# Kernel tuning notes

Measured on AMD Instinct MI355X. Metric: run time of the kernel, lower is better.

The kernel has to match this reference:

```python
import jax, jax.numpy as jnp
import numpy as np

N, E, H, ED, NF, NG = 75000, 150000, 44, 10, 15000, 1500


def _seg_mean(v, idx, n):
    s = jax.ops.segment_sum(v, idx, num_segments=n)
    c = jax.ops.segment_sum(jnp.ones((v.shape[0], 1), v.dtype), idx, num_segments=n)
    return s / jnp.maximum(c, 1.0)


def setup_inputs() -> dict:
    key = jax.random.key(0)
    ks = jax.random.split(key, 26)
    p = lambda k, shape: (jax.random.normal(k, shape, dtype=jnp.float32) * 0.1)
    x = jax.random.normal(ks[0], (N, H), dtype=jnp.float32)
    edge_index = jax.random.randint(ks[1], (2, E), 0, N)
    edge_attr = jax.random.normal(ks[2], (E, ED), dtype=jnp.float32)
    node2frag = (jnp.arange(N) * NF) // N          # sorted, covers all fragments
    frag2graph = (jnp.arange(NF) * NG) // NF       # sorted, covers all graphs
    noise = jax.random.normal(ks[3], (NF, H), dtype=jnp.float32)
    return {
        "x": x, "edge_attr": edge_attr, "noise": noise,
        "W0": p(ks[4], (H, H)), "b0": jnp.zeros((H,)),
        "We1": p(ks[5], (ED, ED)), "be1": jnp.zeros((ED,)),
        "We2": p(ks[6], (ED, H * H)), "be2": jnp.zeros((H * H,)),
        "root": p(ks[7], (H, H)), "conv_b": jnp.zeros((H,)),
        "Wm": p(ks[8], (2 * H, H)), "bm": jnp.zeros((H,)),
        "Wc1": p(ks[9], (H, H)), "bc1": jnp.zeros((H,)),
        "bn_g": jnp.ones((H,)), "bn_b": jnp.zeros((H,)),
        "Wc2": p(ks[10], (H, 1)), "bc2": jnp.zeros((1,)),
        "Wp1": p(ks[11], (H, 256)), "bp1": jnp.zeros((256,)),
        "Wp2": p(ks[12], (256, 128)), "bp2": jnp.zeros((128,)),
        "Wp3": p(ks[13], (128, 1)), "bp3": jnp.zeros((1,)),
        "edge_index": edge_index, "node2frag": node2frag, "frag2graph": frag2graph,
        "n_frags": NF, "n_graphs": NG,
    }


def reference(x, edge_attr, noise, W0, b0, We1, be1, We2, be2, root, conv_b, Wm, bm,
              Wc1, bc1, bn_g, bn_b, Wc2, bc2, Wp1, bp1, Wp2, bp2, Wp3, bp3,
              edge_index, node2frag, frag2graph, n_frags, n_graphs):
    n, h = x.shape
    init = x
    out = jax.nn.relu(x @ W0 + b0)
    # edge-conditioned weight matrices (computed once; edge_attr is fixed)
    ew = (jax.nn.relu(edge_attr @ We1 + be1) @ We2 + be2).reshape(-1, h, h)  # [E,h,h]
    src, dst = edge_index[0], edge_index[1]
    for _ in range(3):  # num_step_message_passing
        msg = jnp.einsum('eh,eho->eo', out[src], ew)               # per-edge matvec
        agg = jax.ops.segment_sum(msg, dst, num_segments=n)        # aggr='add'
        m = jax.nn.relu(agg + out @ root + conv_b)                 # NNConv + relu
        out = jnp.concatenate([m, out], axis=1) @ Wm + bm          # message_layer
    nodef = out + init
    # F.normalize(dim=1)
    nodef = nodef / jnp.maximum(jnp.linalg.norm(nodef, axis=1, keepdims=True), 1e-12)
    frag = _seg_mean(nodef, node2frag, n_frags)                    # global_mean_pool
    # compressor: Linear -> BatchNorm(train stats) -> ReLU -> Linear -> Sigmoid
    z = frag @ Wc1 + bc1
    z = (z - z.mean(0)) / jnp.sqrt(z.var(0) + 1e-5) * bn_g + bn_b
    w = jax.nn.sigmoid(jax.nn.relu(z) @ Wc2 + bc2).squeeze(-1)     # [NF]
    lp = w[:, None]
    ln = 1.0 - lp
    preserve_rate = (w > 0.5).astype(jnp.float32).mean()
    static = jax.lax.stop_gradient(frag)
    cnt = jax.ops.segment_sum(jnp.ones((n_frags,), jnp.float32), frag2graph, num_segments=n_graphs)[:, None]
    gsum = jax.ops.segment_sum(static, frag2graph, num_segments=n_graphs)
    gmean = gsum / jnp.maximum(cnt, 1.0)
    gsq = jax.ops.segment_sum(static * static, frag2graph, num_segments=n_graphs)
    gvar = (gsq - cnt * gmean * gmean) / jnp.maximum(cnt - 1.0, 1.0)  # unbiased (scatter_std)
    gstd = jnp.sqrt(jnp.maximum(gvar, 0.0))
    mean_f = gmean[frag2graph]
    std_f = gstd[frag2graph]
    nmean = lp * frag + ln * mean_f
    nstd = ln * std_f
    noisy = nmean + noise * nstd
    sub = _seg_mean(noisy, frag2graph, n_graphs)
    pred = jax.nn.sigmoid(jax.nn.relu(jax.nn.relu(sub @ Wp1 + bp1) @ Wp2 + bp2) @ Wp3 + bp3)
    eps = 1e-7
    kl = 0.5 * jax.ops.segment_sum((nstd ** 2 / (std_f + eps) ** 2).mean(axis=1), frag2graph, num_segments=n_graphs)[:, None] \
         + jax.ops.segment_sum(((nmean - mean_f) / (std_f + eps)) ** 2, frag2graph, num_segments=n_graphs)
    return pred, kl.mean(), preserve_rate
```

## Files before the change

kernel.cpp:

```cpp
#include <hip/hip_runtime.h>
#include <math.h>

#define NN 75000
#define NE 150000
#define H 44
#define HH 1936
#define EDIM 10
#define NFRAG 15000
#define NGRAPH 1500

typedef const float* __restrict__ cfp;
typedef float* __restrict__ fpt;
typedef const int* __restrict__ cip;
typedef int* __restrict__ ipt;

__device__ __forceinline__ float relu_(float v){ return v > 0.f ? v : 0.f; }
__device__ __forceinline__ float sigmoid_(float v){ return 1.f/(1.f + expf(-v)); }

__global__ __launch_bounds__(256) void k_hist(cip ei, ipt cnt){
    int e = blockIdx.x*256 + threadIdx.x;
    if(e>=NE) return;
    atomicAdd(&cnt[ei[NE+e]], 1);
}

__global__ __launch_bounds__(1024) void k_scan1(cip cnt, ipt incl, ipt bsum){
    __shared__ int sd[1024];
    int i = blockIdx.x*1024 + threadIdx.x;
    int v = (i<NN)? cnt[i] : 0;
    sd[threadIdx.x]=v;
    __syncthreads();
    for(int off=1; off<1024; off<<=1){
        int t = (threadIdx.x>=off)? sd[threadIdx.x-off] : 0;
        __syncthreads();
        sd[threadIdx.x]+=t;
        __syncthreads();
    }
    if(i<NN) incl[i]=sd[threadIdx.x];
    if(threadIdx.x==1023) bsum[blockIdx.x]=sd[1023];
}

__global__ void k_scan2(ipt bsum, int nblk){
    if(threadIdx.x==0 && blockIdx.x==0){
        int run=0;
        for(int b=0;b<nblk;b++){ int t=bsum[b]; bsum[b]=run; run+=t; }
    }
}

__global__ __launch_bounds__(1024) void k_scan3(cip incl, cip bsum, ipt rowptr){
    int i = blockIdx.x*1024 + threadIdx.x;
    if(i==0) rowptr[0]=0;
    if(i<NN) rowptr[i+1] = incl[i] + bsum[i>>10];
}

__global__ __launch_bounds__(256) void k_scatter(cip ei, cip rowptr, ipt cur, ipt eidx){
    int e = blockIdx.x*256 + threadIdx.x;
    if(e>=NE) return;
    int d = ei[NE+e];
    int pos = rowptr[d] + atomicAdd(&cur[d],1);
    eidx[pos]=e;
}

__global__ __launch_bounds__(256) void k_in(cfp x, cfp W0, cfp b0, fpt out){
    __shared__ float sW[HH];
    __shared__ float sb[H];
    for(int i=threadIdx.x;i<HH;i+=256) sW[i]=W0[i];
    if(threadIdx.x<H) sb[threadIdx.x]=b0[threadIdx.x];
    __syncthreads();
    int n = blockIdx.x*256 + threadIdx.x;
    if(n>=NN) return;
    float xv[H];
    const float4* xp = (const float4*)(x + (size_t)n*H);
    #pragma unroll
    for(int i=0;i<11;i++){ float4 v=xp[i]; xv[4*i]=v.x; xv[4*i+1]=v.y; xv[4*i+2]=v.z; xv[4*i+3]=v.w; }
    float acc[H];
    #pragma unroll
    for(int o=0;o<H;o++) acc[o]=sb[o];
    #pragma unroll
    for(int h=0;h<H;h++){
        float xh = xv[h];
        const float4* wr = (const float4*)(sW + h*H);
        #pragma unroll
        for(int o=0;o<11;o++){
            float4 w = wr[o];
            acc[4*o]+=xh*w.x; acc[4*o+1]+=xh*w.y; acc[4*o+2]+=xh*w.z; acc[4*o+3]+=xh*w.w;
        }
    }
    float4* op = (float4*)(out + (size_t)n*H);
    #pragma unroll
    for(int i=0;i<11;i++) op[i] = make_float4(relu_(acc[4*i]),relu_(acc[4*i+1]),relu_(acc[4*i+2]),relu_(acc[4*i+3]));
}

__global__ __launch_bounds__(256) void k_b2(cfp out, cfp be2, fpt b2){
    __shared__ float sB[HH];
    for(int i=threadIdx.x;i<HH;i+=256) sB[i]=be2[i];
    __syncthreads();
    int n = blockIdx.x*256 + threadIdx.x;
    if(n>=NN) return;
    float ov[H];
    const float4* op = (const float4*)(out + (size_t)n*H);
    #pragma unroll
    for(int i=0;i<11;i++){ float4 v=op[i]; ov[4*i]=v.x; ov[4*i+1]=v.y; ov[4*i+2]=v.z; ov[4*i+3]=v.w; }
    float acc[H];
    #pragma unroll
    for(int o=0;o<H;o++) acc[o]=0.f;
    #pragma unroll
    for(int h=0;h<H;h++){
        float oh = ov[h];
        const float4* wr = (const float4*)(sB + h*H);
        #pragma unroll
        for(int o=0;o<11;o++){
            float4 w = wr[o];
            acc[4*o]+=oh*w.x; acc[4*o+1]+=oh*w.y; acc[4*o+2]+=oh*w.z; acc[4*o+3]+=oh*w.w;
        }
    }
    float4* bp = (float4*)(b2 + (size_t)n*H);
    #pragma unroll
    for(int i=0;i<11;i++) bp[i] = make_float4(acc[4*i],acc[4*i+1],acc[4*i+2],acc[4*i+3]);
}

__global__ __launch_bounds__(256) void k_edge(cfp ea, cfp We1, cfp be1, fpt t){
    __shared__ float sW[EDIM*EDIM];
    __shared__ float sb[EDIM];
    if(threadIdx.x<EDIM*EDIM) sW[threadIdx.x]=We1[threadIdx.x];
    if(threadIdx.x<EDIM) sb[threadIdx.x]=be1[threadIdx.x];
    __syncthreads();
    int e = blockIdx.x*256 + threadIdx.x;
    if(e>=NE) return;
    float acc[EDIM];
    #pragma unroll
    for(int j=0;j<EDIM;j++) acc[j]=sb[j];
    #pragma unroll
    for(int k=0;k<EDIM;k++){
        float a = ea[(size_t)e*EDIM + k];
        #pragma unroll
        for(int j=0;j<EDIM;j++) acc[j]+=a*sW[k*EDIM+j];
    }
    #pragma unroll
    for(int j=0;j<EDIM;j++) t[(size_t)e*EDIM+j]=relu_(acc[j]);
}

__global__ __launch_bounds__(256,2) void k_msg2(cfp out, cfp b2, cfp t, cfp We2, cip ei, fpt msgbuf){
    __shared__ float4 sW[EDIM*HH/4];
    const float4* wg = (const float4*)We2;
    for(int i=threadIdx.x;i<EDIM*HH/4;i+=256) sW[i]=wg[i];
    __syncthreads();
    int e0 = blockIdx.x*256 + threadIdx.x;
    if(e0 >= NE/2) return;
    int e1 = e0 + NE/2;
    int s0 = ei[e0], s1 = ei[e1];
    float ov0[H], ov1[H];
    const float4* p0 = (const float4*)(out + (size_t)s0*H);
    const float4* p1 = (const float4*)(out + (size_t)s1*H);
    #pragma unroll
    for(int i=0;i<11;i++){
        float4 a=p0[i]; ov0[4*i]=a.x; ov0[4*i+1]=a.y; ov0[4*i+2]=a.z; ov0[4*i+3]=a.w;
        float4 b=p1[i]; ov1[4*i]=b.x; ov1[4*i+1]=b.y; ov1[4*i+2]=b.z; ov1[4*i+3]=b.w;
    }
    float4 m0[11], m1[11];
    const float4* q0 = (const float4*)(b2 + (size_t)s0*H);
    const float4* q1 = (const float4*)(b2 + (size_t)s1*H);
    #pragma unroll
    for(int i=0;i<11;i++){ m0[i]=q0[i]; m1[i]=q1[i]; }
    for(int k=0;k<EDIM;k++){
        float t0 = t[(size_t)e0*EDIM + k];
        float t1 = t[(size_t)e1*EDIM + k];
        const float4* wrow = &sW[k*(HH/4)];
        #pragma unroll
        for(int h=0;h<H;h++){
            float z0 = t0*ov0[h];
            float z1 = t1*ov1[h];
            #pragma unroll
            for(int o=0;o<11;o++){
                float4 w = wrow[h*11+o];
                m0[o].x+=z0*w.x; m0[o].y+=z0*w.y; m0[o].z+=z0*w.z; m0[o].w+=z0*w.w;
                m1[o].x+=z1*w.x; m1[o].y+=z1*w.y; m1[o].z+=z1*w.z; m1[o].w+=z1*w.w;
            }
        }
    }
    float4* w0 = (float4*)(msgbuf + (size_t)e0*H);
    float4* w1 = (float4*)(msgbuf + (size_t)e1*H);
    #pragma unroll
    for(int o=0;o<11;o++){ w0[o]=m0[o]; w1[o]=m1[o]; }
}

__global__ __launch_bounds__(256,2) void k_comb(cfp out, cfp msgbuf, cip rowptr, cip eidx,
                                                cfp root, cfp conv_b, cfp Wm, cfp bm, fpt out_nxt){
    __shared__ float sR[HH];
    __shared__ float sM[2*HH];
    __shared__ float scb[H];
    __shared__ float sbm[H];
    for(int i=threadIdx.x;i<HH;i+=256) sR[i]=root[i];
    for(int i=threadIdx.x;i<2*HH;i+=256) sM[i]=Wm[i];
    if(threadIdx.x<H){ scb[threadIdx.x]=conv_b[threadIdx.x]; sbm[threadIdx.x]=bm[threadIdx.x]; }
    __syncthreads();
    int n = blockIdx.x*256 + threadIdx.x;
    if(n>=NN) return;
    float m[H];
    #pragma unroll
    for(int o=0;o<H;o++) m[o]=scb[o];
    int st = rowptr[n], en = rowptr[n+1];
    for(int j=st;j<en;j++){
        int e = eidx[j];
        const float4* mp = (const float4*)(msgbuf + (size_t)e*H);
        #pragma unroll
        for(int i=0;i<11;i++){
            float4 v=mp[i];
            m[4*i]+=v.x; m[4*i+1]+=v.y; m[4*i+2]+=v.z; m[4*i+3]+=v.w;
        }
    }
    float ov[H];
    const float4* op = (const float4*)(out + (size_t)n*H);
    #pragma unroll
    for(int i=0;i<11;i++){ float4 v=op[i]; ov[4*i]=v.x; ov[4*i+1]=v.y; ov[4*i+2]=v.z; ov[4*i+3]=v.w; }
    #pragma unroll
    for(int h=0;h<H;h++){
        float oh = ov[h];
        const float4* wr = (const float4*)(sR + h*H);
        #pragma unroll
        for(int o=0;o<11;o++){
            float4 w=wr[o];
            m[4*o]+=oh*w.x; m[4*o+1]+=oh*w.y; m[4*o+2]+=oh*w.z; m[4*o+3]+=oh*w.w;
        }
    }
    #pragma unroll
    for(int o=0;o<H;o++) m[o]=relu_(m[o]);
    float no[H];
    #pragma unroll
    for(int o=0;o<H;o++) no[o]=sbm[o];
    #pragma unroll
    for(int h=0;h<H;h++){
        float mh = m[h];
        float oh = ov[h];
        const float4* w1 = (const float4*)(sM + h*H);
        const float4* w2 = (const float4*)(sM + (H+h)*H);
        #pragma unroll
        for(int o=0;o<11;o++){
            float4 a=w1[o], b=w2[o];
            no[4*o]+=mh*a.x+oh*b.x; no[4*o+1]+=mh*a.y+oh*b.y; no[4*o+2]+=mh*a.z+oh*b.z; no[4*o+3]+=mh*a.w+oh*b.w;
        }
    }
    float4* np_ = (float4*)(out_nxt + (size_t)n*H);
    #pragma unroll
    for(int i=0;i<11;i++) np_[i]=make_float4(no[4*i],no[4*i+1],no[4*i+2],no[4*i+3]);
}

__global__ __launch_bounds__(256) void k_frag(cfp out, cfp x, cfp Wc1, cfp bc1,
                                              fpt frag, fpt z, fpt colstat){
    __shared__ float sW[HH];
    __shared__ float sb[H];
    for(int i=threadIdx.x;i<HH;i+=256) sW[i]=Wc1[i];
    if(threadIdx.x<H) sb[threadIdx.x]=bc1[threadIdx.x];
    __syncthreads();
    int f = blockIdx.x*256 + threadIdx.x;
    bool valid = f < NFRAG;
    int fc = valid ? f : NFRAG-1;
    float fr[H];
    #pragma unroll
    for(int o=0;o<H;o++) fr[o]=0.f;
    for(int j=0;j<5;j++){
        int n = 5*fc + j;
        float v[H]; float ss=0.f;
        const float4* op=(const float4*)(out + (size_t)n*H);
        const float4* xp=(const float4*)(x + (size_t)n*H);
        #pragma unroll
        for(int i=0;i<11;i++){
            float4 a=op[i], b=xp[i];
            v[4*i]=a.x+b.x; v[4*i+1]=a.y+b.y; v[4*i+2]=a.z+b.z; v[4*i+3]=a.w+b.w;
        }
        #pragma unroll
        for(int o=0;o<H;o++) ss+=v[o]*v[o];
        float inv = 1.f/fmaxf(sqrtf(ss),1e-12f);
        #pragma unroll
        for(int o=0;o<H;o++) fr[o]+=v[o]*inv;
    }
    #pragma unroll
    for(int o=0;o<H;o++) fr[o]*=0.2f;
    float zr[H];
    #pragma unroll
    for(int o=0;o<H;o++) zr[o]=sb[o];
    #pragma unroll
    for(int h=0;h<H;h++){
        float fh = fr[h];
        const float4* wr=(const float4*)(sW + h*H);
        #pragma unroll
        for(int o=0;o<11;o++){
            float4 w=wr[o];
            zr[4*o]+=fh*w.x; zr[4*o+1]+=fh*w.y; zr[4*o+2]+=fh*w.z; zr[4*o+3]+=fh*w.w;
        }
    }
    if(valid){
        float4* fw=(float4*)(frag+(size_t)f*H);
        float4* zw=(float4*)(z+(size_t)f*H);
        #pragma unroll
        for(int i=0;i<11;i++){
            fw[i]=make_float4(fr[4*i],fr[4*i+1],fr[4*i+2],fr[4*i+3]);
            zw[i]=make_float4(zr[4*i],zr[4*i+1],zr[4*i+2],zr[4*i+3]);
        }
    }
    #pragma unroll
    for(int o=0;o<H;o++){
        float s = valid ? zr[o] : 0.f;
        float q = s*s;
        #pragma unroll
        for(int dlt=32;dlt>0;dlt>>=1){ s+=__shfl_xor(s,dlt); q+=__shfl_xor(q,dlt); }
        if((threadIdx.x&63)==0){ atomicAdd(colstat+o,s); atomicAdd(colstat+H+o,q); }
    }
}

__global__ __launch_bounds__(256) void k_bnw(cfp z, cfp colstat, cfp bng, cfp bnb, cfp Wc2, cfp bc2, fpt w, fpt pres){
    int f = blockIdx.x*256 + threadIdx.x;
    bool valid = f < NFRAG;
    int fc = valid ? f : NFRAG-1;
    float s = 0.f;
    #pragma unroll
    for(int o=0;o<H;o++){
        float mean = colstat[o]*(1.f/NFRAG);
        float var  = colstat[H+o]*(1.f/NFRAG) - mean*mean;
        float zb = (z[(size_t)fc*H+o]-mean)*rsqrtf(var+1e-5f)*bng[o]+bnb[o];
        s += relu_(zb)*Wc2[o];
    }
    float wv = sigmoid_(s + bc2[0]);
    if(valid) w[f]=wv;
    unsigned long long msk = __ballot(valid && (wv > 0.5f));
    if((threadIdx.x&63)==0) atomicAdd(pres,(float)__popcll(msk));
}

__global__ __launch_bounds__(64) void k_graph(cfp frag, cfp w, cfp noise, fpt sub, fpt klg){
    int g = blockIdx.x;
    int o = threadIdx.x;
    bool act = o < H;
    int oc = act ? o : 0;
    float frv[10];
    #pragma unroll
    for(int j=0;j<10;j++) frv[j] = act ? frag[(size_t)(10*g+j)*H + oc] : 0.f;
    float gs=0.f, gq=0.f;
    #pragma unroll
    for(int j=0;j<10;j++){ gs+=frv[j]; gq+=frv[j]*frv[j]; }
    float gmean = gs*0.1f;
    float gvar  = (gq - 10.f*gmean*gmean)*(1.f/9.f);
    float gstd  = sqrtf(fmaxf(gvar,0.f));
    float se    = gstd + 1e-7f;
    float c     = act ? (gstd/se)*(gstd/se) : 0.f;
    float C = c;
    #pragma unroll
    for(int dlt=32;dlt>0;dlt>>=1) C+=__shfl_xor(C,dlt);
    float subacc=0.f, B=0.f, Sln=0.f;
    #pragma unroll
    for(int j=0;j<10;j++){
        float lp = w[10*g+j];
        float ln = 1.f-lp;
        Sln += ln*ln;
        float nm = lp*frv[j] + ln*gmean;
        float ns = ln*gstd;
        float ny = nm + (act ? noise[(size_t)(10*g+j)*H + oc] : 0.f)*ns;
        subacc += ny;
        float dd = (nm-gmean)/se;
        B += dd*dd;
    }
    if(act) sub[(size_t)g*H+o] = subacc*0.1f;
    float Bv = act ? B : 0.f;
    #pragma unroll
    for(int dlt=32;dlt>0;dlt>>=1) Bv+=__shfl_xor(Bv,dlt);
    if(o==0) klg[g] = 0.5f*C*Sln + Bv;
}

__global__ __launch_bounds__(256) void k_pred(cfp sub, cfp Wp1, cfp bp1, cfp Wp2, cfp bp2,
                                              cfp Wp3, cfp bp3, fpt outp){
    __shared__ float ssub[H];
    __shared__ float sh1[256];
    __shared__ float sh2[128];
    int g = blockIdx.x; int tid = threadIdx.x;
    if(tid<H) ssub[tid] = sub[(size_t)g*H+tid];
    __syncthreads();
    float a = bp1[tid];
    for(int o=0;o<H;o++) a += ssub[o]*Wp1[(size_t)o*256+tid];
    sh1[tid]=relu_(a);
    __syncthreads();
    if(tid<128){
        float b = bp2[tid];
        for(int i=0;i<256;i++) b += sh1[i]*Wp2[(size_t)i*128+tid];
        sh2[tid]=relu_(b);
    }
    __syncthreads();
    if(tid<64){
        float s = sh2[tid]*Wp3[tid] + sh2[tid+64]*Wp3[tid+64];
        #pragma unroll
        for(int dlt=32;dlt>0;dlt>>=1) s+=__shfl_xor(s,dlt);
        if(tid==0) outp[g]=sigmoid_(s+bp3[0]);
    }
}

__global__ void k_final(cfp klg, cfp pres, fpt outp){
    float s = 0.f;
    for(int i=threadIdx.x;i<NGRAPH;i+=256) s+=klg[i];
    __shared__ float red[4];
    #pragma unroll
    for(int dlt=32;dlt>0;dlt>>=1) s+=__shfl_xor(s,dlt);
    int wid = threadIdx.x>>6;
    if((threadIdx.x&63)==0) red[wid]=s;
    __syncthreads();
    if(threadIdx.x==0){
        float tot = red[0]+red[1]+red[2]+red[3];
        outp[NGRAPH]   = tot/(float)(NGRAPH*H);
        outp[NGRAPH+1] = pres[0]/(float)NFRAG;
    }
}

extern "C" void kernel_launch(void* const* d_in, const int* in_sizes, int n_in,
                              void* d_out, int out_size, void* d_ws, size_t ws_size,
                              hipStream_t stream) {
    (void)in_sizes; (void)n_in; (void)out_size; (void)ws_size;
    const float* x        =(const float*)d_in[0];
    const float* edge_attr=(const float*)d_in[1];
    const float* noise    =(const float*)d_in[2];
    const float* W0       =(const float*)d_in[3];
    const float* b0       =(const float*)d_in[4];
    const float* We1      =(const float*)d_in[5];
    const float* be1      =(const float*)d_in[6];
    const float* We2      =(const float*)d_in[7];
    const float* be2      =(const float*)d_in[8];
    const float* root     =(const float*)d_in[9];
    const float* conv_b   =(const float*)d_in[10];
    const float* Wm       =(const float*)d_in[11];
    const float* bm       =(const float*)d_in[12];
    const float* Wc1      =(const float*)d_in[13];
    const float* bc1      =(const float*)d_in[14];
    const float* bng      =(const float*)d_in[15];
    const float* bnb      =(const float*)d_in[16];
    const float* Wc2      =(const float*)d_in[17];
    const float* bc2      =(const float*)d_in[18];
    const float* Wp1      =(const float*)d_in[19];
    const float* bp1      =(const float*)d_in[20];
    const float* Wp2      =(const float*)d_in[21];
    const float* bp2      =(const float*)d_in[22];
    const float* Wp3      =(const float*)d_in[23];
    const float* bp3      =(const float*)d_in[24];
    const int*   ei       =(const int*)d_in[25];

    float* ws = (float*)d_ws;
    const size_t NH = (size_t)NN*H;
    float* out_a  = ws;
    float* out_b  = out_a + NH;
    float* b2_a   = out_b + NH;
    float* b2_b   = b2_a + NH;
    float* tbuf   = b2_b + NH;
    float* msgbuf = tbuf + (size_t)NE*EDIM;
    float* frag   = msgbuf + (size_t)NE*H;
    float* zbuf   = frag + (size_t)NFRAG*H;
    float* wv     = zbuf + (size_t)NFRAG*H;
    float* sub    = wv + NFRAG;
    float* klg    = sub + (size_t)NGRAPH*H;
    int*   rowptr = (int*)(klg + NGRAPH);
    int*   eidx   = rowptr + (NN+1);
    int*   bsum   = eidx + NE;
    int*   incl   = bsum + 128;
    int*   cnt    = incl + NN;
    int*   cur    = cnt + NN;
    float* colstat= (float*)(cur + NN);
    float* pres   = colstat + 2*H;

    hipMemsetAsync(cnt, 0, (size_t)(2*NN + 2*H + 8)*sizeof(float), stream);

    const int nb_n = (NN + 255)/256;
    const int nb_e = (NE + 255)/256;
    const int nb_h = (NE/2 + 255)/256;
    const int nb_f = (NFRAG + 255)/256;
    const int nblk = (NN + 1023)/1024;

    k_hist   <<<nb_e,256,0,stream>>>(ei, cnt);
    k_scan1  <<<nblk,1024,0,stream>>>(cnt, incl, bsum);
    k_scan2  <<<1,64,0,stream>>>(bsum, nblk);
    k_scan3  <<<nblk,1024,0,stream>>>(incl, bsum, rowptr);
    k_scatter<<<nb_e,256,0,stream>>>(ei, rowptr, cur, eidx);

    k_in  <<<nb_n,256,0,stream>>>(x, W0, b0, out_a);
    k_b2  <<<nb_n,256,0,stream>>>(out_a, be2, b2_a);
    k_edge<<<nb_e,256,0,stream>>>(edge_attr, We1, be1, tbuf);

    float* cur_o = out_a; float* cur_b = b2_a;
    float* nxt_o = out_b; float* nxt_b = b2_b;
    for(int it=0; it<3; ++it){
        k_msg2<<<nb_h,256,0,stream>>>(cur_o, cur_b, tbuf, We2, ei, msgbuf);
        k_comb<<<nb_n,256,0,stream>>>(cur_o, msgbuf, rowptr, eidx, root, conv_b, Wm, bm, nxt_o);
        if(it<2) k_b2<<<nb_n,256,0,stream>>>(nxt_o, be2, nxt_b);
        float* tp;
        tp=cur_o; cur_o=nxt_o; nxt_o=tp;
        tp=cur_b; cur_b=nxt_b; nxt_b=tp;
    }

    k_frag <<<nb_f,256,0,stream>>>(cur_o, x, Wc1, bc1, frag, zbuf, colstat);
    k_bnw  <<<nb_f,256,0,stream>>>(zbuf, colstat, bng, bnb, Wc2, bc2, wv, pres);
    k_graph<<<NGRAPH,64,0,stream>>>(frag, wv, noise, sub, klg);
    k_pred <<<NGRAPH,256,0,stream>>>(sub, Wp1, bp1, Wp2, bp2, Wp3, bp3, (float*)d_out);
    k_final<<<1,256,0,stream>>>(klg, pres, (float*)d_out);
}
```

Before: 1.410 ms.

## Restructure node/edge matmuls with padded rows, LDS-transposed tiles, and output-group split

Node feature rows are padded to 48 floats, in four 11-wide groups of 12, and the per-thread 44x44 dense loops in k_b2, k_msg and k_comb become block-cooperative kernels. Each block stages its tile transposed in LDS. Each wavefront computes one 11-output group for four (or two) rows, reading weights from global/scalar memory instead of per-thread register rows. The aim is lower register pressure and better reuse of the weight stream. k_frag is also split so that normalization, fragment pooling and the Wc1 matmul are done cooperatively in LDS, with 4 threads per fragment. The cost is extra LDS traffic, more synchronisation and padded memory footprint.

```diff
diff --git a/kernel.cpp b/kernel.cpp
--- a/kernel.cpp
+++ b/kernel.cpp
@@ -4,7 +4,7 @@
 #define NN 75000
 #define NE 150000
 #define H 44
-#define HH 1936
+#define HS 48
 #define EDIM 10
 #define NFRAG 15000
 #define NGRAPH 1500
@@ -14,8 +14,8 @@
 typedef const int* __restrict__ cip;
 typedef int* __restrict__ ipt;
 
-__device__ __forceinline__ float relu_(float v){ return v > 0.f ? v : 0.f; }
-__device__ __forceinline__ float sigmoid_(float v){ return 1.f/(1.f + expf(-v)); }
+__device__ __forceinline__ float relu_(float v){ return v>0.f?v:0.f; }
+__device__ __forceinline__ float sigmoid_(float v){ return 1.f/(1.f+expf(-v)); }
 
 __global__ __launch_bounds__(256) void k_hist(cip ei, ipt cnt){
     int e = blockIdx.x*256 + threadIdx.x;
@@ -61,9 +61,9 @@
 }
 
 __global__ __launch_bounds__(256) void k_in(cfp x, cfp W0, cfp b0, fpt out){
-    __shared__ float sW[HH];
+    __shared__ float sW[H*H];
     __shared__ float sb[H];
-    for(int i=threadIdx.x;i<HH;i+=256) sW[i]=W0[i];
+    for(int i=threadIdx.x;i<H*H;i+=256) sW[i]=W0[i];
     if(threadIdx.x<H) sb[threadIdx.x]=b0[threadIdx.x];
     __syncthreads();
     int n = blockIdx.x*256 + threadIdx.x;
@@ -85,37 +85,60 @@
             acc[4*o]+=xh*w.x; acc[4*o+1]+=xh*w.y; acc[4*o+2]+=xh*w.z; acc[4*o+3]+=xh*w.w;
         }
     }
-    float4* op = (float4*)(out + (size_t)n*H);
-    #pragma unroll
-    for(int i=0;i<11;i++) op[i] = make_float4(relu_(acc[4*i]),relu_(acc[4*i+1]),relu_(acc[4*i+2]),relu_(acc[4*i+3]));
-}
-
-__global__ __launch_bounds__(256) void k_b2(cfp out, cfp be2, fpt b2){
-    __shared__ float sB[HH];
-    for(int i=threadIdx.x;i<HH;i+=256) sB[i]=be2[i];
-    __syncthreads();
-    int n = blockIdx.x*256 + threadIdx.x;
-    if(n>=NN) return;
-    float ov[H];
-    const float4* op = (const float4*)(out + (size_t)n*H);
-    #pragma unroll
-    for(int i=0;i<11;i++){ float4 v=op[i]; ov[4*i]=v.x; ov[4*i+1]=v.y; ov[4*i+2]=v.z; ov[4*i+3]=v.w; }
-    float acc[H];
-    #pragma unroll
-    for(int o=0;o<H;o++) acc[o]=0.f;
+    #pragma unroll
+    for(int o=0;o<H;o++) acc[o]=relu_(acc[o]);
+    float* row = out + (size_t)n*HS;
+    #pragma unroll
+    for(int s=0;s<4;s++){
+        float4* p=(float4*)(row + s*12);
+        p[0]=make_float4(acc[11*s+0],acc[11*s+1],acc[11*s+2],acc[11*s+3]);
+        p[1]=make_float4(acc[11*s+4],acc[11*s+5],acc[11*s+6],acc[11*s+7]);
+        p[2]=make_float4(acc[11*s+8],acc[11*s+9],acc[11*s+10],0.f);
+    }
+}
+
+#define NB2 256
+__global__ __launch_bounds__(256,3) void k_b2(cfp out, cfp be2, fpt b2){
+    __shared__ float ovT[HS*NB2];
+    int tid=threadIdx.x, lane=tid&63;
+    int og = __builtin_amdgcn_readfirstlane(tid>>6);
+    size_t base=(size_t)blockIdx.x*NB2;
+    { size_t n=base+tid; size_t nc = n<NN? n : NN-1;
+      const float4* orow=(const float4*)(out + nc*HS);
+      #pragma unroll
+      for(int i=0;i<12;i++){ float4 v=orow[i];
+        ovT[(4*i+0)*NB2+tid]=v.x; ovT[(4*i+1)*NB2+tid]=v.y;
+        ovT[(4*i+2)*NB2+tid]=v.z; ovT[(4*i+3)*NB2+tid]=v.w; }
+    }
+    __syncthreads();
+    float m[4][11];
+    #pragma unroll
+    for(int j=0;j<4;j++)
+        #pragma unroll
+        for(int o=0;o<11;o++) m[j][o]=0.f;
+    const float* wog = be2 + og*11;
     #pragma unroll
     for(int h=0;h<H;h++){
-        float oh = ov[h];
-        const float4* wr = (const float4*)(sB + h*H);
+        int hl = h + h/11;
+        const float4* ovp=(const float4*)(ovT + hl*NB2 + lane*4);
+        float4 ov=ovp[0];
         #pragma unroll
         for(int o=0;o<11;o++){
-            float4 w = wr[o];
-            acc[4*o]+=oh*w.x; acc[4*o+1]+=oh*w.y; acc[4*o+2]+=oh*w.z; acc[4*o+3]+=oh*w.w;
-        }
-    }
-    float4* bp = (float4*)(b2 + (size_t)n*H);
-    #pragma unroll
-    for(int i=0;i<11;i++) bp[i] = make_float4(acc[4*i],acc[4*i+1],acc[4*i+2],acc[4*i+3]);
+            float w = wog[h*H+o];
+            m[0][o]+=ov.x*w; m[1][o]+=ov.y*w; m[2][o]+=ov.z*w; m[3][o]+=ov.w*w;
+        }
+    }
+    size_t n0 = base + (size_t)lane*4;
+    #pragma unroll
+    for(int j=0;j<4;j++){
+        size_t n=n0+j;
+        if(n<NN){
+            float4* p=(float4*)(b2 + n*HS + og*12);
+            p[0]=make_float4(m[j][0],m[j][1],m[j][2],m[j][3]);
+            p[1]=make_float4(m[j][4],m[j][5],m[j][6],m[j][7]);
+            p[2]=make_float4(m[j][8],m[j][9],m[j][10],0.f);
+        }
+    }
 }
 
 __global__ __launch_bounds__(256) void k_edge(cfp ea, cfp We1, cfp be1, fpt t){
@@ -139,171 +162,230 @@
     for(int j=0;j<EDIM;j++) t[(size_t)e*EDIM+j]=relu_(acc[j]);
 }
 
-__global__ __launch_bounds__(256,2) void k_msg2(cfp out, cfp b2, cfp t, cfp We2, cip ei, fpt msgbuf){
-    __shared__ float4 sW[EDIM*HH/4];
-    const float4* wg = (const float4*)We2;
-    for(int i=threadIdx.x;i<EDIM*HH/4;i+=256) sW[i]=wg[i];
-    __syncthreads();
-    int e0 = blockIdx.x*256 + threadIdx.x;
-    if(e0 >= NE/2) return;
-    int e1 = e0 + NE/2;
-    int s0 = ei[e0], s1 = ei[e1];
-    float ov0[H], ov1[H];
-    const float4* p0 = (const float4*)(out + (size_t)s0*H);
-    const float4* p1 = (const float4*)(out + (size_t)s1*H);
-    #pragma unroll
-    for(int i=0;i<11;i++){
-        float4 a=p0[i]; ov0[4*i]=a.x; ov0[4*i+1]=a.y; ov0[4*i+2]=a.z; ov0[4*i+3]=a.w;
-        float4 b=p1[i]; ov1[4*i]=b.x; ov1[4*i+1]=b.y; ov1[4*i+2]=b.z; ov1[4*i+3]=b.w;
-    }
-    float4 m0[11], m1[11];
-    const float4* q0 = (const float4*)(b2 + (size_t)s0*H);
-    const float4* q1 = (const float4*)(b2 + (size_t)s1*H);
-    #pragma unroll
-    for(int i=0;i<11;i++){ m0[i]=q0[i]; m1[i]=q1[i]; }
+#define EBM 256
+__global__ __launch_bounds__(256,2) void k_msg(cfp out, cfp b2, cfp t, cfp We2, cip ei, fpt msg){
+    __shared__ float ovT[HS*EBM];
+    __shared__ float tT[EDIM*EBM];
+    int tid=threadIdx.x, lane=tid&63;
+    int og = __builtin_amdgcn_readfirstlane(tid>>6);
+    size_t base=(size_t)blockIdx.x*EBM;
+    { size_t e=base+tid; size_t ec = e<NE? e : NE-1;
+      int s = ei[ec];
+      const float4* orow=(const float4*)(out + (size_t)s*HS);
+      #pragma unroll
+      for(int i=0;i<12;i++){ float4 v=orow[i];
+        ovT[(4*i+0)*EBM+tid]=v.x; ovT[(4*i+1)*EBM+tid]=v.y;
+        ovT[(4*i+2)*EBM+tid]=v.z; ovT[(4*i+3)*EBM+tid]=v.w; }
+      const float2* trow=(const float2*)(t + ec*EDIM);
+      #pragma unroll
+      for(int i=0;i<5;i++){ float2 v=trow[i]; tT[(2*i+0)*EBM+tid]=v.x; tT[(2*i+1)*EBM+tid]=v.y; }
+    }
+    __syncthreads();
+    size_t e0 = base + (size_t)lane*4;
+    int srcj[4];
+    #pragma unroll
+    for(int j=0;j<4;j++){ size_t e=e0+j; srcj[j]=ei[e<NE? e : NE-1]; }
+    float m[4][11];
+    #pragma unroll
+    for(int j=0;j<4;j++){
+        const float4* br=(const float4*)(b2 + (size_t)srcj[j]*HS + og*12);
+        float4 A=br[0],B=br[1],C=br[2];
+        m[j][0]=A.x; m[j][1]=A.y; m[j][2]=A.z; m[j][3]=A.w;
+        m[j][4]=B.x; m[j][5]=B.y; m[j][6]=B.z; m[j][7]=B.w;
+        m[j][8]=C.x; m[j][9]=C.y; m[j][10]=C.z;
+    }
+    const float* wog = We2 + og*11;
     for(int k=0;k<EDIM;k++){
-        float t0 = t[(size_t)e0*EDIM + k];
-        float t1 = t[(size_t)e1*EDIM + k];
-        const float4* wrow = &sW[k*(HH/4)];
+        const float4* tp=(const float4*)(tT + k*EBM + lane*4);
+        float4 t4=tp[0];
+        const float* wk = wog + k*(H*H);
         #pragma unroll
         for(int h=0;h<H;h++){
-            float z0 = t0*ov0[h];
-            float z1 = t1*ov1[h];
+            int hl = h + h/11;
+            const float4* ovp=(const float4*)(ovT + hl*EBM + lane*4);
+            float4 ov=ovp[0];
+            float z0=t4.x*ov.x, z1=t4.y*ov.y, z2=t4.z*ov.z, z3=t4.w*ov.w;
             #pragma unroll
             for(int o=0;o<11;o++){
-                float4 w = wrow[h*11+o];
-                m0[o].x+=z0*w.x; m0[o].y+=z0*w.y; m0[o].z+=z0*w.z; m0[o].w+=z0*w.w;
-                m1[o].x+=z1*w.x; m1[o].y+=z1*w.y; m1[o].z+=z1*w.z; m1[o].w+=z1*w.w;
+                float w = wk[h*H+o];
+                m[0][o]+=z0*w; m[1][o]+=z1*w; m[2][o]+=z2*w; m[3][o]+=z3*w;
             }
         }
     }
-    float4* w0 = (float4*)(msgbuf + (size_t)e0*H);
-    float4* w1 = (float4*)(msgbuf + (size_t)e1*H);
-    #pragma unroll
-    for(int o=0;o<11;o++){ w0[o]=m0[o]; w1[o]=m1[o]; }
-}
-
-__global__ __launch_bounds__(256,2) void k_comb(cfp out, cfp msgbuf, cip rowptr, cip eidx,
+    #pragma unroll
+    for(int j=0;j<4;j++){
+        size_t e=e0+j;
+        if(e<NE){
+            float4* p=(float4*)(msg + e*HS + og*12);
+            p[0]=make_float4(m[j][0],m[j][1],m[j][2],m[j][3]);
+            p[1]=make_float4(m[j][4],m[j][5],m[j][6],m[j][7]);
+            p[2]=make_float4(m[j][8],m[j][9],m[j][10],0.f);
+        }
+    }
+}
+
+#define NBC 128
+__global__ __launch_bounds__(256,3) void k_comb(cfp out, cfp msg, cip rowptr, cip eidx,
                                                 cfp root, cfp conv_b, cfp Wm, cfp bm, fpt out_nxt){
-    __shared__ float sR[HH];
-    __shared__ float sM[2*HH];
-    __shared__ float scb[H];
-    __shared__ float sbm[H];
-    for(int i=threadIdx.x;i<HH;i+=256) sR[i]=root[i];
-    for(int i=threadIdx.x;i<2*HH;i+=256) sM[i]=Wm[i];
-    if(threadIdx.x<H){ scb[threadIdx.x]=conv_b[threadIdx.x]; sbm[threadIdx.x]=bm[threadIdx.x]; }
-    __syncthreads();
-    int n = blockIdx.x*256 + threadIdx.x;
-    if(n>=NN) return;
-    float m[H];
-    #pragma unroll
-    for(int o=0;o<H;o++) m[o]=scb[o];
-    int st = rowptr[n], en = rowptr[n+1];
-    for(int j=st;j<en;j++){
-        int e = eidx[j];
-        const float4* mp = (const float4*)(msgbuf + (size_t)e*H);
-        #pragma unroll
-        for(int i=0;i<11;i++){
-            float4 v=mp[i];
-            m[4*i]+=v.x; m[4*i+1]+=v.y; m[4*i+2]+=v.z; m[4*i+3]+=v.w;
-        }
-    }
-    float ov[H];
-    const float4* op = (const float4*)(out + (size_t)n*H);
-    #pragma unroll
-    for(int i=0;i<11;i++){ float4 v=op[i]; ov[4*i]=v.x; ov[4*i+1]=v.y; ov[4*i+2]=v.z; ov[4*i+3]=v.w; }
+    __shared__ float ovT[HS*NBC];
+    __shared__ float mT[HS*NBC];
+    int tid=threadIdx.x, lane=tid&63;
+    int og = __builtin_amdgcn_readfirstlane(tid>>6);
+    size_t base=(size_t)blockIdx.x*NBC;
+    { int nl=tid>>1, half=tid&1;
+      size_t n=base+nl; size_t nc = n<NN? n : NN-1;
+      const float4* orow=(const float4*)(out + nc*HS + half*24);
+      #pragma unroll
+      for(int i=0;i<6;i++){ float4 v=orow[i];
+        ovT[(half*24+4*i+0)*NBC+nl]=v.x; ovT[(half*24+4*i+1)*NBC+nl]=v.y;
+        ovT[(half*24+4*i+2)*NBC+nl]=v.z; ovT[(half*24+4*i+3)*NBC+nl]=v.w; }
+    }
+    __syncthreads();
+    size_t n0 = base + (size_t)lane*2;
+    float m[2][11];
+    #pragma unroll
+    for(int j=0;j<2;j++)
+        #pragma unroll
+        for(int o=0;o<11;o++) m[j][o]=conv_b[og*11+o];
+    #pragma unroll
+    for(int j=0;j<2;j++){
+        size_t n=n0+j; size_t nc = n<NN? n : NN-1;
+        int st=rowptr[nc], en=rowptr[nc+1];
+        for(int idx=st; idx<en; idx++){
+            int e=eidx[idx];
+            const float4* p=(const float4*)(msg + (size_t)e*HS + og*12);
+            float4 A=p[0],B=p[1],C=p[2];
+            m[j][0]+=A.x; m[j][1]+=A.y; m[j][2]+=A.z; m[j][3]+=A.w;
+            m[j][4]+=B.x; m[j][5]+=B.y; m[j][6]+=B.z; m[j][7]+=B.w;
+            m[j][8]+=C.x; m[j][9]+=C.y; m[j][10]+=C.z;
+        }
+    }
+    const float* rog = root + og*11;
     #pragma unroll
     for(int h=0;h<H;h++){
-        float oh = ov[h];
-        const float4* wr = (const float4*)(sR + h*H);
+        int hl = h + h/11;
+        const float2* ovp=(const float2*)(ovT + hl*NBC + lane*2);
+        float2 ov=ovp[0];
         #pragma unroll
         for(int o=0;o<11;o++){
-            float4 w=wr[o];
-            m[4*o]+=oh*w.x; m[4*o+1]+=oh*w.y; m[4*o+2]+=oh*w.z; m[4*o+3]+=oh*w.w;
-        }
-    }
-    #pragma unroll
-    for(int o=0;o<H;o++) m[o]=relu_(m[o]);
-    float no[H];
-    #pragma unroll
-    for(int o=0;o<H;o++) no[o]=sbm[o];
+            float w = rog[h*H+o];
+            m[0][o]+=ov.x*w; m[1][o]+=ov.y*w;
+        }
+    }
+    #pragma unroll
+    for(int j=0;j<2;j++)
+        #pragma unroll
+        for(int o=0;o<11;o++) m[j][o]=relu_(m[j][o]);
+    #pragma unroll
+    for(int j=0;j<2;j++)
+        #pragma unroll
+        for(int o=0;o<11;o++) mT[(og*12+o)*NBC + lane*2+j]=m[j][o];
+    __syncthreads();
+    float no[2][11];
+    #pragma unroll
+    for(int j=0;j<2;j++)
+        #pragma unroll
+        for(int o=0;o<11;o++) no[j][o]=bm[og*11+o];
+    const float* wmog = Wm + og*11;
     #pragma unroll
     for(int h=0;h<H;h++){
-        float mh = m[h];
-        float oh = ov[h];
-        const float4* w1 = (const float4*)(sM + h*H);
-        const float4* w2 = (const float4*)(sM + (H+h)*H);
+        int hl = h + h/11;
+        const float2* mp=(const float2*)(mT + hl*NBC + lane*2);
+        const float2* ovp=(const float2*)(ovT + hl*NBC + lane*2);
+        float2 mh=mp[0], ov=ovp[0];
         #pragma unroll
         for(int o=0;o<11;o++){
-            float4 a=w1[o], b=w2[o];
-            no[4*o]+=mh*a.x+oh*b.x; no[4*o+1]+=mh*a.y+oh*b.y; no[4*o+2]+=mh*a.z+oh*b.z; no[4*o+3]+=mh*a.w+oh*b.w;
-        }
-    }
-    float4* np_ = (float4*)(out_nxt + (size_t)n*H);
-    #pragma unroll
-    for(int i=0;i<11;i++) np_[i]=make_float4(no[4*i],no[4*i+1],no[4*i+2],no[4*i+3]);
-}
-
-__global__ __launch_bounds__(256) void k_frag(cfp out, cfp x, cfp Wc1, cfp bc1,
-                                              fpt frag, fpt z, fpt colstat){
-    __shared__ float sW[HH];
-    __shared__ float sb[H];
-    for(int i=threadIdx.x;i<HH;i+=256) sW[i]=Wc1[i];
-    if(threadIdx.x<H) sb[threadIdx.x]=bc1[threadIdx.x];
-    __syncthreads();
-    int f = blockIdx.x*256 + threadIdx.x;
-    bool valid = f < NFRAG;
-    int fc = valid ? f : NFRAG-1;
-    float fr[H];
-    #pragma unroll
-    for(int o=0;o<H;o++) fr[o]=0.f;
-    for(int j=0;j<5;j++){
-        int n = 5*fc + j;
-        float v[H]; float ss=0.f;
-        const float4* op=(const float4*)(out + (size_t)n*H);
+            float a = wmog[h*H+o];
+            float b = wmog[(H+h)*H+o];
+            no[0][o]+=mh.x*a+ov.x*b;
+            no[1][o]+=mh.y*a+ov.y*b;
+        }
+    }
+    #pragma unroll
+    for(int j=0;j<2;j++){
+        size_t n=n0+j;
+        if(n<NN){
+            float4* p=(float4*)(out_nxt + n*HS + og*12);
+            p[0]=make_float4(no[j][0],no[j][1],no[j][2],no[j][3]);
+            p[1]=make_float4(no[j][4],no[j][5],no[j][6],no[j][7]);
+            p[2]=make_float4(no[j][8],no[j][9],no[j][10],0.f);
+        }
+    }
+}
+
+__global__ __launch_bounds__(256,2) void k_frag(cfp out, cfp x, cfp Wc1, cfp bc1,
+                                                fpt frag, fpt z, fpt colstat){
+    __shared__ float nd[250*45];
+    __shared__ float frS[50*45];
+    __shared__ float sW[H*H];
+    int tid=threadIdx.x;
+    for(int i=tid;i<H*H;i+=256) sW[i]=Wc1[i];
+    if(tid<250){
+        int n = blockIdx.x*250 + tid;
+        float v[H];
         const float4* xp=(const float4*)(x + (size_t)n*H);
         #pragma unroll
-        for(int i=0;i<11;i++){
-            float4 a=op[i], b=xp[i];
-            v[4*i]=a.x+b.x; v[4*i+1]=a.y+b.y; v[4*i+2]=a.z+b.z; v[4*i+3]=a.w+b.w;
-        }
+        for(int i=0;i<11;i++){ float4 a=xp[i]; v[4*i]=a.x; v[4*i+1]=a.y; v[4*i+2]=a.z; v[4*i+3]=a.w; }
+        const float4* orow=(const float4*)(out + (size_t)n*HS);
+        #pragma unroll
+        for(int s=0;s<4;s++){
+            float4 A=orow[3*s+0],B=orow[3*s+1],C=orow[3*s+2];
+            v[11*s+0]+=A.x; v[11*s+1]+=A.y; v[11*s+2]+=A.z; v[11*s+3]+=A.w;
+            v[11*s+4]+=B.x; v[11*s+5]+=B.y; v[11*s+6]+=B.z; v[11*s+7]+=B.w;
+            v[11*s+8]+=C.x; v[11*s+9]+=C.y; v[11*s+10]+=C.z;
+        }
+        float ss=0.f;
         #pragma unroll
         for(int o=0;o<H;o++) ss+=v[o]*v[o];
         float inv = 1.f/fmaxf(sqrtf(ss),1e-12f);
         #pragma unroll
-        for(int o=0;o<H;o++) fr[o]+=v[o]*inv;
-    }
-    #pragma unroll
-    for(int o=0;o<H;o++) fr[o]*=0.2f;
-    float zr[H];
-    #pragma unroll
-    for(int o=0;o<H;o++) zr[o]=sb[o];
-    #pragma unroll
+        for(int o=0;o<H;o++) nd[tid*45+o]=v[o]*inv;
+    }
+    __syncthreads();
+    if(tid<50){
+        float fr[H];
+        #pragma unroll
+        for(int o=0;o<H;o++) fr[o]=0.f;
+        for(int j=0;j<5;j++){
+            int r=tid*5+j;
+            #pragma unroll
+            for(int o=0;o<H;o++) fr[o]+=nd[r*45+o];
+        }
+        #pragma unroll
+        for(int o=0;o<H;o++){ fr[o]*=0.2f; frS[tid*45+o]=fr[o]; }
+        int f = blockIdx.x*50 + tid;
+        float4* fw=(float4*)(frag + (size_t)f*H);
+        #pragma unroll
+        for(int i=0;i<11;i++) fw[i]=make_float4(fr[4*i],fr[4*i+1],fr[4*i+2],fr[4*i+3]);
+    }
+    __syncthreads();
+    int fl=tid>>2, q=tid&3;
+    int flc = fl<50? fl : 0;
+    bool fv = fl<50;
+    float zr[11];
+    #pragma unroll
+    for(int o=0;o<11;o++) zr[o]=bc1[q*11+o];
     for(int h=0;h<H;h++){
-        float fh = fr[h];
-        const float4* wr=(const float4*)(sW + h*H);
-        #pragma unroll
-        for(int o=0;o<11;o++){
-            float4 w=wr[o];
-            zr[4*o]+=fh*w.x; zr[4*o+1]+=fh*w.y; zr[4*o+2]+=fh*w.z; zr[4*o+3]+=fh*w.w;
-        }
-    }
-    if(valid){
-        float4* fw=(float4*)(frag+(size_t)f*H);
-        float4* zw=(float4*)(z+(size_t)f*H);
-        #pragma unroll
-        for(int i=0;i<11;i++){
-            fw[i]=make_float4(fr[4*i],fr[4*i+1],fr[4*i+2],fr[4*i+3]);
-            zw[i]=make_float4(zr[4*i],zr[4*i+1],zr[4*i+2],zr[4*i+3]);
-        }
-    }
-    #pragma unroll
-    for(int o=0;o<H;o++){
-        float s = valid ? zr[o] : 0.f;
-        float q = s*s;
-        #pragma unroll
-        for(int dlt=32;dlt>0;dlt>>=1){ s+=__shfl_xor(s,dlt); q+=__shfl_xor(q,dlt); }
-        if((threadIdx.x&63)==0){ atomicAdd(colstat+o,s); atomicAdd(colstat+H+o,q); }
+        float fh = frS[flc*45+h];
+        #pragma unroll
+        for(int o=0;o<11;o++) zr[o]+=fh*sW[h*H+q*11+o];
+    }
+    #pragma unroll
+    for(int o=0;o<11;o++) if(!fv) zr[o]=0.f;
+    if(fv){
+        int f = blockIdx.x*50 + fl;
+        #pragma unroll
+        for(int o=0;o<11;o++) z[(size_t)f*H + q*11+o]=zr[o];
+    }
+    #pragma unroll
+    for(int o=0;o<11;o++){
+        float s=zr[o], sq=zr[o]*zr[o];
+        #pragma unroll
+        for(int d=4;d<64;d<<=1){ s+=__shfl_xor(s,d); sq+=__shfl_xor(sq,d); }
+        if((tid&63)<4){
+            atomicAdd(colstat + q*11+o, s);
+            atomicAdd(colstat + H + q*11+o, sq);
+        }
     }
 }
 
@@ -438,14 +520,14 @@
     const int*   ei       =(const int*)d_in[25];
 
     float* ws = (float*)d_ws;
-    const size_t NH = (size_t)NN*H;
+    const size_t NHS = (size_t)NN*HS;
     float* out_a  = ws;
-    float* out_b  = out_a + NH;
-    float* b2_a   = out_b + NH;
-    float* b2_b   = b2_a + NH;
-    float* tbuf   = b2_b + NH;
+    float* out_b  = out_a + NHS;
+    float* b2_a   = out_b + NHS;
+    float* b2_b   = b2_a + NHS;
+    float* tbuf   = b2_b + NHS;
     float* msgbuf = tbuf + (size_t)NE*EDIM;
-    float* frag   = msgbuf + (size_t)NE*H;
+    float* frag   = msgbuf + (size_t)NE*HS;
     float* zbuf   = frag + (size_t)NFRAG*H;
     float* wv     = zbuf + (size_t)NFRAG*H;
     float* sub    = wv + NFRAG;
@@ -461,11 +543,11 @@
 
     hipMemsetAsync(cnt, 0, (size_t)(2*NN + 2*H + 8)*sizeof(float), stream);
 
-    const int nb_n = (NN + 255)/256;
-    const int nb_e = (NE + 255)/256;
-    const int nb_h = (NE/2 + 255)/256;
-    const int nb_f = (NFRAG + 255)/256;
-    const int nblk = (NN + 1023)/1024;
+    const int nb_n  = (NN + 255)/256;
+    const int nb_e  = (NE + 255)/256;
+    const int nb_f  = (NFRAG + 255)/256;
+    const int nblk  = (NN + 1023)/1024;
+    const int nb_c  = (NN + NBC-1)/NBC;
 
     k_hist   <<<nb_e,256,0,stream>>>(ei, cnt);
     k_scan1  <<<nblk,1024,0,stream>>>(cnt, incl, bsum);
@@ -480,15 +562,15 @@
     float* cur_o = out_a; float* cur_b = b2_a;
     float* nxt_o = out_b; float* nxt_b = b2_b;
     for(int it=0; it<3; ++it){
-        k_msg2<<<nb_h,256,0,stream>>>(cur_o, cur_b, tbuf, We2, ei, msgbuf);
-        k_comb<<<nb_n,256,0,stream>>>(cur_o, msgbuf, rowptr, eidx, root, conv_b, Wm, bm, nxt_o);
+        k_msg <<<nb_e,256,0,stream>>>(cur_o, cur_b, tbuf, We2, ei, msgbuf);
+        k_comb<<<nb_c,256,0,stream>>>(cur_o, msgbuf, rowptr, eidx, root, conv_b, Wm, bm, nxt_o);
         if(it<2) k_b2<<<nb_n,256,0,stream>>>(nxt_o, be2, nxt_b);
         float* tp;
         tp=cur_o; cur_o=nxt_o; nxt_o=tp;
         tp=cur_b; cur_b=nxt_b; nxt_b=tp;
     }
 
-    k_frag <<<nb_f,256,0,stream>>>(cur_o, x, Wc1, bc1, frag, zbuf, colstat);
+    k_frag <<<300,256,0,stream>>>(cur_o, x, Wc1, bc1, frag, zbuf, colstat);
     k_bnw  <<<nb_f,256,0,stream>>>(zbuf, colstat, bng, bnb, Wc2, bc2, wv, pres);
     k_graph<<<NGRAPH,64,0,stream>>>(frag, wv, noise, sub, klg);
     k_pred <<<NGRAPH,256,0,stream>>>(sub, Wp1, bp1, Wp2, bp2, Wp3, bp3, (float*)d_out);
```

New measurement: 1.676 ms. +18.9%, slower.
